# Performance work log

Hardware: AMD Instinct MI355X
Metric: run time of the kernel (lower is better)

The kernel has to match this reference:

```python
import jax, jax.numpy as jnp
import numpy as np

E = 512   # embed_dim
S = 16    # stat_dim
B = 2048  # batch
K = 64    # neighbors


def setup_inputs() -> dict:
    key = jax.random.key(0)
    ks = jax.random.split(key, 12)
    std_s1 = 1.0 / np.sqrt(3 * E + S)
    std_s2 = 1.0 / np.sqrt(E)
    std_p1 = 1.0 / np.sqrt(E + S)
    return {
        "query": jax.random.normal(ks[0], (B, E), jnp.float32),
        "condition": jax.random.normal(ks[1], (B, E), jnp.float32),
        "neighbors": jax.random.normal(ks[2], (B, K, E), jnp.float32),
        "neighbor_stats": jax.random.uniform(ks[3], (B, K, S), jnp.float32),
        # scorer: Linear(3E+S -> E), GELU, Linear(E -> 1)
        "sw1": jax.random.uniform(ks[4], (3 * E + S, E), jnp.float32, -std_s1, std_s1),
        "sb1": jax.random.uniform(ks[5], (E,), jnp.float32, -std_s1, std_s1),
        "sw2": jax.random.uniform(ks[6], (E, 1), jnp.float32, -std_s2, std_s2),
        "sb2": jax.random.uniform(ks[7], (1,), jnp.float32, -std_s2, std_s2),
        "sim_alpha": jnp.float32(1.0),
        # proj: Linear(E+S -> E), GELU, Linear(E -> E)
        "pw1": jax.random.uniform(ks[8], (E + S, E), jnp.float32, -std_p1, std_p1),
        "pb1": jax.random.uniform(ks[9], (E,), jnp.float32, -std_p1, std_p1),
        "pw2": jax.random.uniform(ks[10], (E, E), jnp.float32, -std_s2, std_s2),
        "pb2": jax.random.uniform(ks[11], (E,), jnp.float32, -std_s2, std_s2),
    }


def _gelu(x):
    return jax.nn.gelu(x, approximate=False)  # torch default GELU is exact erf


def reference(query, condition, neighbors, neighbor_stats,
              sw1, sb1, sw2, sb2, sim_alpha, pw1, pb1, pw2, pb2):
    b, k, e = neighbors.shape
    # broadcast query/condition over k and concat -> [B, K, 3E+S]
    q_rep = jnp.broadcast_to(query[:, None, :], (b, k, e))
    c_rep = jnp.broadcast_to(condition[:, None, :], (b, k, e))
    scorer_in = jnp.concatenate([q_rep, c_rep, neighbors, neighbor_stats], axis=-1)
    h = _gelu(scorer_in @ sw1 + sb1)          # dropout is identity in eval
    logits = (h @ sw2 + sb2)[..., 0]           # [B, K]
    sim_scores = neighbor_stats[..., -1]       # stat_dim > 0
    logits = logits + sim_alpha * sim_scores
    attn = jax.nn.softmax(logits, axis=-1)     # [B, K]
    nb_cat = jnp.concatenate([neighbors, neighbor_stats], axis=-1)  # [B, K, E+S]
    mixed = jnp.einsum('bk,bkd->bd', attn, nb_cat)
    out = _gelu(mixed @ pw1 + pb1) @ pw2 + pb2  # [B, E]
    return out, attn
```

## Files before the change

kernel.cpp:

```cpp
#include <hip/hip_runtime.h>

typedef _Float16 half_t;
typedef _Float16 half2_t __attribute__((ext_vector_type(2)));
typedef _Float16 half4_t __attribute__((ext_vector_type(4)));
typedef _Float16 half8_t __attribute__((ext_vector_type(8)));
typedef float floatx4 __attribute__((ext_vector_type(4)));
typedef float floatx16 __attribute__((ext_vector_type(16)));

#define NE 512
#define NS 16
#define NBATCH 2048
#define NK 64
#define AS 552

__device__ __forceinline__ float gelu_erf(float x) {
    float z = x * 0.70710678118654752440f;
    float az2 = z * z;
    float az = __builtin_fabsf(z);
    float t = __builtin_amdgcn_rcpf(__builtin_fmaf(0.3275911f, az, 1.0f));
    float p = __builtin_fmaf(1.061405429f, t, -1.453152027f);
    p = __builtin_fmaf(p, t, 1.421413741f);
    p = __builtin_fmaf(p, t, -0.284496736f);
    p = __builtin_fmaf(p, t, 0.254829592f);
    p = p * t;
    float e = __expf(-az2);
    float erfa = __builtin_fmaf(-p, e, 1.0f);
    unsigned int u = __float_as_uint(erfa) ^ (__float_as_uint(z) & 0x80000000u);
    return 0.5f * x * (1.0f + __uint_as_float(u));
}

__device__ __forceinline__ half4_t cvt4(float4 v) {
    return (half4_t){(half_t)v.x, (half_t)v.y, (half_t)v.z, (half_t)v.w};
}

__device__ __forceinline__ float colreduce16(const float (&x)[16], int lnb) {
    float y[8];
#pragma unroll
    for (int i = 0; i < 8; ++i) {
        float keep = (lnb & 1) ? x[2 * i + 1] : x[2 * i];
        float send = (lnb & 1) ? x[2 * i] : x[2 * i + 1];
        y[i] = keep + __shfl_xor(send, 1, 64);
    }
    float z[4];
#pragma unroll
    for (int i = 0; i < 4; ++i) {
        float keep = (lnb & 2) ? y[2 * i + 1] : y[2 * i];
        float send = (lnb & 2) ? y[2 * i] : y[2 * i + 1];
        z[i] = keep + __shfl_xor(send, 2, 64);
    }
    float u[2];
#pragma unroll
    for (int i = 0; i < 2; ++i) {
        float keep = (lnb & 4) ? z[2 * i + 1] : z[2 * i];
        float send = (lnb & 4) ? z[2 * i] : z[2 * i + 1];
        u[i] = keep + __shfl_xor(send, 4, 64);
    }
    float keep = (lnb & 8) ? u[1] : u[0];
    float send = (lnb & 8) ? u[0] : u[1];
    float v = keep + __shfl_xor(send, 8, 64);
    v += __shfl_xor(v, 16, 64);
    return v;
}

__device__ void pack_w_body(const float* __restrict__ src, half_t* __restrict__ dst,
                            int Ksrc, int t, int nb0, half_t* tile) {
    int tid = threadIdx.x;
#pragma unroll
    for (int i = 0; i < 8; ++i) {
        int idx = tid + i * 256;
        int kk = idx >> 6, np = idx & 63;
        int k = t * 32 + kk;
        float v = (k < Ksrc) ? src[(size_t)k * NE + nb0 + np] : 0.0f;
        tile[kk * 68 + np] = (half_t)v;
    }
    __syncthreads();
#pragma unroll
    for (int i = 0; i < 8; ++i) {
        int idx = tid + i * 256;
        int np = idx >> 5, kk = idx & 31;
        dst[((size_t)t * NE + nb0 + np) * 32 + kk] = tile[kk * 68 + np];
    }
}

__device__ void pack_w32_body(const float* __restrict__ src, half_t* __restrict__ dst,
                              int Ksrc, int t, int nb0, half_t* tile) {
    int tid = threadIdx.x;
#pragma unroll
    for (int i = 0; i < 4; ++i) {
        int idx = tid + i * 256;
        int kk = idx >> 6, n = idx & 63;
        int k = t * 16 + kk;
        float v = (k < Ksrc) ? src[(size_t)k * NE + nb0 + n] : 0.0f;
        tile[kk * 68 + n] = (half_t)v;
    }
    __syncthreads();
    int n = threadIdx.x >> 2, q = threadIdx.x & 3;
    half4_t h = {tile[(q * 4) * 68 + n], tile[(q * 4 + 1) * 68 + n],
                 tile[(q * 4 + 2) * 68 + n], tile[(q * 4 + 3) * 68 + n]};
    *(half4_t*)&dst[((size_t)t * NE + nb0 + n) * 16 + q * 4] = h;
}

__global__ __launch_bounds__(256) void pack_all(
    const float* __restrict__ sw1, const float* __restrict__ pw1,
    const float* __restrict__ pw2, half_t* __restrict__ Wq,
    half_t* __restrict__ Wns, half_t* __restrict__ Wp1, half_t* __restrict__ Wp2) {
    __shared__ half_t tile[32 * 68];
    int bx = blockIdx.x;
    if (bx < 256) {
        pack_w_body(sw1, Wq, 1024, bx >> 3, (bx & 7) * 64, tile);
    } else if (bx < 520) {
        int b2 = bx - 256;
        pack_w32_body(sw1 + (size_t)1024 * NE, Wns, 528, b2 >> 3, (b2 & 7) * 64, tile);
    } else if (bx < 656) {
        int b3 = bx - 520;
        pack_w_body(pw1, Wp1, 528, b3 >> 3, (b3 & 7) * 64, tile);
    } else {
        int b4 = bx - 656;
        pack_w_body(pw2, Wp2, 512, b4 >> 3, (b4 & 7) * 64, tile);
    }
}

__global__ __launch_bounds__(512) void qc_kernel(const float* __restrict__ q,
                                                 const float* __restrict__ c,
                                                 const half_t* __restrict__ Wq,
                                                 const float* __restrict__ sb1,
                                                 float* __restrict__ qcb) {
    constexpr int AS1 = 1032;
    __shared__ __align__(16) half_t A1[16 * AS1];
    int b0 = (blockIdx.x >> 1) * 16;
    int nh = (blockIdx.x & 1) * 256;
    int tid = threadIdx.x;
#pragma unroll
    for (int i = 0; i < 8; ++i) {
        int f = tid + i * 512;
        int row = f >> 8;
        int c4 = f & 255;
        const float* srcp = (c4 < 128) ? (q + (size_t)(b0 + row) * NE + c4 * 4)
                                       : (c + (size_t)(b0 + row) * NE + (c4 - 128) * 4);
        float4 v = *(const float4*)srcp;
        *(half4_t*)&A1[row * AS1 + c4 * 4] = cvt4(v);
    }
    __syncthreads();
    int w = tid >> 6, l = tid & 63, lg = l >> 4, ln = l & 15;
    floatx4 acc[2] = { {0,0,0,0}, {0,0,0,0} };
    for (int t = 0; t < 32; ++t) {
        half8_t a = *(const half8_t*)&A1[ln * AS1 + t * 32 + 8 * lg];
#pragma unroll
        for (int ni = 0; ni < 2; ++ni) {
            int n = nh + w * 32 + ni * 16 + ln;
            half8_t bf = *(const half8_t*)(Wq + ((size_t)t * NE + n) * 32 + 8 * lg);
            acc[ni] = __builtin_amdgcn_mfma_f32_16x16x32_f16(a, bf, acc[ni], 0, 0, 0);
        }
    }
#pragma unroll
    for (int ni = 0; ni < 2; ++ni) {
        int col = nh + w * 32 + ni * 16 + ln;
        float bias = sb1[col];
#pragma unroll
        for (int r = 0; r < 4; ++r) {
            int row = 4 * lg + r;
            qcb[(size_t)(b0 + row) * NE + col] = acc[ni][r] + bias;
        }
    }
}

__global__ __launch_bounds__(512, 4) void main_kernel(
    const float* __restrict__ neighbors, const float* __restrict__ stats,
    const half_t* __restrict__ Wns, const float* __restrict__ qcb,
    const float* __restrict__ sw2, const float* __restrict__ sb2,
    const float* __restrict__ alpha, float* __restrict__ attn_out,
    half_t* __restrict__ mixed) {
    __shared__ __align__(16) half_t A[64 * AS];
    __shared__ float Llds[64][17];
    __shared__ float attn_s[8][64];

    int b = blockIdx.x;
    int tid = threadIdx.x;
    const float* nb = neighbors + (size_t)b * NK * NE;
    const float* st = stats + (size_t)b * NK * NS;

    int r0 = tid >> 5;
    int c4 = tid & 31;
    int w = tid >> 6;
    int l = tid & 63, ln = l & 31, hi = l >> 5;
    const half_t* Abase = A + ln * AS + 8 * hi;
    const half_t* Wb = Wns + ((size_t)(w * 32 + ln)) * 16 + 8 * hi;

    float4 s0, s1, s2, s3, sst;
    float qv1, w21, qv2, w22;
    {
        float4 p0 = *(const float4*)(nb + (size_t)(r0) * NE + 4 * c4);
        float4 p1 = *(const float4*)(nb + (size_t)(r0 + 16) * NE + 4 * c4);
        float4 p2 = *(const float4*)(nb + (size_t)(r0 + 32) * NE + 4 * c4);
        float4 p3 = *(const float4*)(nb + (size_t)(r0 + 48) * NE + 4 * c4);
        __builtin_amdgcn_sched_barrier(0);
        s0 = *(const float4*)(nb + (size_t)(r0) * NE + 128 + 4 * c4);
        s1 = *(const float4*)(nb + (size_t)(r0 + 16) * NE + 128 + 4 * c4);
        s2 = *(const float4*)(nb + (size_t)(r0 + 32) * NE + 128 + 4 * c4);
        s3 = *(const float4*)(nb + (size_t)(r0 + 48) * NE + 128 + 4 * c4);
        qv1 = qcb[(size_t)b * NE + w * 32 + ln];
        w21 = sw2[w * 32 + ln];
        qv2 = qcb[(size_t)b * NE + 256 + w * 32 + ln];
        w22 = sw2[256 + w * 32 + ln];
        __builtin_amdgcn_sched_barrier(0);
        *(half4_t*)&A[(r0) * AS + 4 * c4] = cvt4(p0);
        *(half4_t*)&A[(r0 + 16) * AS + 4 * c4] = cvt4(p1);
        *(half4_t*)&A[(r0 + 32) * AS + 4 * c4] = cvt4(p2);
        *(half4_t*)&A[(r0 + 48) * AS + 4 * c4] = cvt4(p3);
    }
    asm volatile("s_waitcnt lgkmcnt(0)" ::: "memory");
    __builtin_amdgcn_sched_barrier(0);
    __builtin_amdgcn_s_barrier();
    __builtin_amdgcn_sched_barrier(0);

    floatx16 acc0 = {0,0,0,0,0,0,0,0,0,0,0,0,0,0,0,0};
    floatx16 acc1 = {0,0,0,0,0,0,0,0,0,0,0,0,0,0,0,0};

#pragma unroll 1
    for (int ch = 0; ch < 4; ++ch) {
        half8_t bfr[8];
#pragma unroll
        for (int s8 = 0; s8 < 8; ++s8)
            bfr[s8] = *(const half8_t*)(Wb + (size_t)(ch * 8 + s8) * 8192);
        __builtin_amdgcn_sched_barrier(0);
        float4 n0, n1, n2, n3;
        if (ch < 2) {
            n0 = *(const float4*)(nb + (size_t)(r0) * NE + (ch + 2) * 128 + 4 * c4);
            n1 = *(const float4*)(nb + (size_t)(r0 + 16) * NE + (ch + 2) * 128 + 4 * c4);
            n2 = *(const float4*)(nb + (size_t)(r0 + 32) * NE + (ch + 2) * 128 + 4 * c4);
            n3 = *(const float4*)(nb + (size_t)(r0 + 48) * NE + (ch + 2) * 128 + 4 * c4);
        } else if (ch == 2) {
            if (tid < 256)
                sst = *(const float4*)(st + (tid >> 2) * NS + (tid & 3) * 4);
        }
        __builtin_amdgcn_sched_barrier(0);
#pragma unroll
        for (int s8 = 0; s8 < 8; ++s8) {
            int col = ch * 128 + s8 * 16;
            half8_t a0 = *(const half8_t*)&Abase[col];
            half8_t a1 = *(const half8_t*)&Abase[32 * AS + col];
            acc0 = __builtin_amdgcn_mfma_f32_32x32x16_f16(a0, bfr[s8], acc0, 0, 0, 0);
            acc1 = __builtin_amdgcn_mfma_f32_32x32x16_f16(a1, bfr[s8], acc1, 0, 0, 0);
        }
        if (ch < 3) {
            *(half4_t*)&A[(r0) * AS + (ch + 1) * 128 + 4 * c4] = cvt4(s0);
            *(half4_t*)&A[(r0 + 16) * AS + (ch + 1) * 128 + 4 * c4] = cvt4(s1);
            *(half4_t*)&A[(r0 + 32) * AS + (ch + 1) * 128 + 4 * c4] = cvt4(s2);
            *(half4_t*)&A[(r0 + 48) * AS + (ch + 1) * 128 + 4 * c4] = cvt4(s3);
            s0 = n0; s1 = n1; s2 = n2; s3 = n3;
        } else {
            if (tid < 256)
                *(half4_t*)&A[(tid >> 2) * AS + 512 + (tid & 3) * 4] = cvt4(sst);
        }
        asm volatile("s_waitcnt lgkmcnt(0)" ::: "memory");
        __builtin_amdgcn_sched_barrier(0);
        __builtin_amdgcn_s_barrier();
        __builtin_amdgcn_sched_barrier(0);
    }
    {
        half8_t bfa = *(const half8_t*)(Wb + (size_t)32 * 8192);
        half8_t a0 = *(const half8_t*)&Abase[512];
        half8_t a1 = *(const half8_t*)&Abase[32 * AS + 512];
        acc0 = __builtin_amdgcn_mfma_f32_32x32x16_f16(a0, bfa, acc0, 0, 0, 0);
        acc1 = __builtin_amdgcn_mfma_f32_32x32x16_f16(a1, bfa, acc1, 0, 0, 0);
    }

    const half_t* Wb2 = Wb + 4096;
    half8_t pA0 = *(const half8_t*)(Wb2);
    half8_t pB0 = *(const half8_t*)(Wb2 + 8192);
    half8_t pA1 = *(const half8_t*)(Wb2 + 2 * 8192);
    half8_t pB1 = *(const half8_t*)(Wb2 + 3 * 8192);
    __builtin_amdgcn_sched_barrier(0);

    {
        float g0[16], g1[16];
#pragma unroll
        for (int r = 0; r < 16; ++r) {
            g0[r] = gelu_erf(acc0[r] + qv1) * w21;
            g1[r] = gelu_erf(acc1[r] + qv1) * w21;
        }
        float rA = colreduce16(g0, ln);
        float rB = colreduce16(g1, ln);
        if (ln < 16) {
            int row = (ln & 3) + 8 * (ln >> 2) + 4 * hi;
            Llds[row][w] = rA;
            Llds[32 + row][w] = rB;
        }
    }

    acc0 = (floatx16){0,0,0,0,0,0,0,0,0,0,0,0,0,0,0,0};
    acc1 = (floatx16){0,0,0,0,0,0,0,0,0,0,0,0,0,0,0,0};
#pragma unroll 1
    for (int t2 = 0; t2 < 16; ++t2) {
        int tn = 2 * t2 + 4;
        if (tn > 32) tn = 32;
        int tn1 = tn + 1;
        if (tn1 > 32) tn1 = 32;
        half8_t nA = *(const half8_t*)(Wb2 + (size_t)tn * 8192);
        half8_t nB = *(const half8_t*)(Wb2 + (size_t)tn1 * 8192);
        int col = t2 * 32;
        half8_t a0 = *(const half8_t*)&Abase[col];
        half8_t a1 = *(const half8_t*)&Abase[32 * AS + col];
        acc0 = __builtin_amdgcn_mfma_f32_32x32x16_f16(a0, pA0, acc0, 0, 0, 0);
        acc1 = __builtin_amdgcn_mfma_f32_32x32x16_f16(a1, pA0, acc1, 0, 0, 0);
        half8_t a0b = *(const half8_t*)&Abase[col + 16];
        half8_t a1b = *(const half8_t*)&Abase[32 * AS + col + 16];
        acc0 = __builtin_amdgcn_mfma_f32_32x32x16_f16(a0b, pB0, acc0, 0, 0, 0);
        acc1 = __builtin_amdgcn_mfma_f32_32x32x16_f16(a1b, pB0, acc1, 0, 0, 0);
        pA0 = pA1; pB0 = pB1; pA1 = nA; pB1 = nB;
    }
    {
        half8_t a0 = *(const half8_t*)&Abase[512];
        half8_t a1 = *(const half8_t*)&Abase[32 * AS + 512];
        acc0 = __builtin_amdgcn_mfma_f32_32x32x16_f16(a0, pA0, acc0, 0, 0, 0);
        acc1 = __builtin_amdgcn_mfma_f32_32x32x16_f16(a1, pA0, acc1, 0, 0, 0);
    }

    {
        float g0[16], g1[16];
#pragma unroll
        for (int r = 0; r < 16; ++r) {
            g0[r] = gelu_erf(acc0[r] + qv2) * w22;
            g1[r] = gelu_erf(acc1[r] + qv2) * w22;
        }
        float rA = colreduce16(g0, ln);
        float rB = colreduce16(g1, ln);
        if (ln < 16) {
            int row = (ln & 3) + 8 * (ln >> 2) + 4 * hi;
            Llds[row][8 + w] = rA;
            Llds[32 + row][8 + w] = rB;
        }
    }
    __syncthreads();

    {
        int k = l;
        float lsum = 0.0f;
#pragma unroll
        for (int j = 0; j < 16; ++j) lsum += Llds[k][j];
        float sim = st[k * NS + (NS - 1)];
        float logit = lsum + sb2[0] + alpha[0] * sim;
        float mx = logit;
#pragma unroll
        for (int m = 1; m < 64; m <<= 1) mx = fmaxf(mx, __shfl_xor(mx, m, 64));
        float e = __expf(logit - mx);
        float s = e;
#pragma unroll
        for (int m = 1; m < 64; m <<= 1) s += __shfl_xor(s, m, 64);
        float at = e / s;
        attn_s[w][k] = at;
        if (w == 0) attn_out[(size_t)b * NK + k] = at;
    }

    if (tid < 264) {
        int c0 = 2 * tid;
        float m0 = 0.0f, m1 = 0.0f;
#pragma unroll 8
        for (int k = 0; k < NK; ++k) {
            half2_t v = *(const half2_t*)&A[k * AS + c0];
            float aw = attn_s[w][k];
            m0 += aw * (float)v[0];
            m1 += aw * (float)v[1];
        }
        *(half2_t*)&mixed[(size_t)b * AS + c0] = (half2_t){(half_t)m0, (half_t)m1};
    } else if (tid < 270) {
        int z = tid - 264;
        half4_t hz = {};
        *(half4_t*)&mixed[(size_t)b * AS + 528 + 4 * z] = hz;
    }
}

__global__ __launch_bounds__(1024) void proj_kernel(
    const half_t* __restrict__ mixedp, const half_t* __restrict__ Wp1,
    const half_t* __restrict__ Wp2, const float* __restrict__ pb1,
    const float* __restrict__ pb2, float* __restrict__ out) {
    constexpr int AS3 = AS;
    __shared__ __align__(16) half_t A1[16 * AS3];
    int b0 = blockIdx.x * 16;
    int tid = threadIdx.x;
    const uint4* src = (const uint4*)(mixedp + (size_t)b0 * AS3);
    for (int i = tid; i < 1104; i += 1024) ((uint4*)A1)[i] = src[i];
    __syncthreads();

    int w = tid >> 6, l = tid & 63, lg = l >> 4, ln = l & 15;
    floatx4 acc[2] = { {0,0,0,0}, {0,0,0,0} };
    for (int t = 0; t < 17; ++t) {
        half8_t a = *(const half8_t*)&A1[ln * AS3 + t * 32 + 8 * lg];
#pragma unroll
        for (int ni = 0; ni < 2; ++ni) {
            int n = w * 32 + ni * 16 + ln;
            half8_t bf = *(const half8_t*)(Wp1 + ((size_t)t * NE + n) * 32 + 8 * lg);
            acc[ni] = __builtin_amdgcn_mfma_f32_16x16x32_f16(a, bf, acc[ni], 0, 0, 0);
        }
    }
    __syncthreads();
#pragma unroll
    for (int ni = 0; ni < 2; ++ni) {
        int col = w * 32 + ni * 16 + ln;
        float bias = pb1[col];
#pragma unroll
        for (int r = 0; r < 4; ++r) {
            int row = 4 * lg + r;
            A1[row * AS3 + col] = (half_t)gelu_erf(acc[ni][r] + bias);
        }
    }
    __syncthreads();
    floatx4 acc2[2] = { {0,0,0,0}, {0,0,0,0} };
    for (int t = 0; t < 16; ++t) {
        half8_t a = *(const half8_t*)&A1[ln * AS3 + t * 32 + 8 * lg];
#pragma unroll
        for (int ni = 0; ni < 2; ++ni) {
            int n = w * 32 + ni * 16 + ln;
            half8_t bf = *(const half8_t*)(Wp2 + ((size_t)t * NE + n) * 32 + 8 * lg);
            acc2[ni] = __builtin_amdgcn_mfma_f32_16x16x32_f16(a, bf, acc2[ni], 0, 0, 0);
        }
    }
#pragma unroll
    for (int ni = 0; ni < 2; ++ni) {
        int col = w * 32 + ni * 16 + ln;
        float bias = pb2[col];
#pragma unroll
        for (int r = 0; r < 4; ++r)
            out[(size_t)(b0 + 4 * lg + r) * NE + col] = acc2[ni][r] + bias;
    }
}

extern "C" void kernel_launch(void* const* d_in, const int* in_sizes, int n_in,
                              void* d_out, int out_size, void* d_ws, size_t ws_size,
                              hipStream_t stream) {
    (void)in_sizes; (void)n_in; (void)out_size; (void)ws_size;
    const float* q     = (const float*)d_in[0];
    const float* c     = (const float*)d_in[1];
    const float* nb    = (const float*)d_in[2];
    const float* st    = (const float*)d_in[3];
    const float* sw1   = (const float*)d_in[4];
    const float* sb1   = (const float*)d_in[5];
    const float* sw2   = (const float*)d_in[6];
    const float* sb2   = (const float*)d_in[7];
    const float* alpha = (const float*)d_in[8];
    const float* pw1   = (const float*)d_in[9];
    const float* pb1   = (const float*)d_in[10];
    const float* pw2   = (const float*)d_in[11];
    const float* pb2   = (const float*)d_in[12];

    char* ws = (char*)d_ws;
    half_t* Wq  = (half_t*)(ws + 0);
    half_t* Wns = (half_t*)(ws + 1048576);
    half_t* Wp1 = (half_t*)(ws + 1605632);
    half_t* Wp2 = (half_t*)(ws + 2162688);
    float*  qcb = (float*)(ws + 2686976);
    half_t* mix = (half_t*)(ws + 6881280);

    float* outp  = (float*)d_out;
    float* attnp = outp + (size_t)NBATCH * NE;

    pack_all<<<784, 256, 0, stream>>>(sw1, pw1, pw2, Wq, Wns, Wp1, Wp2);
    qc_kernel<<<256, 512, 0, stream>>>(q, c, Wq, sb1, qcb);
    main_kernel<<<2048, 512, 0, stream>>>(nb, st, Wns, qcb, sw2, sb2, alpha, attnp, mix);
    proj_kernel<<<128, 1024, 0, stream>>>(mix, Wp1, Wp2, pb1, pb2, outp);
}
```

Before: 171.0 us.

## Double-buffer neighbor chunks in LDS and re-stream neighbors to cut LDS footprint

Replaces the full 64x552 half tile in shared memory with two 128-column chunk buffers plus a small stats buffer, and raises the launch-bounds minimum from 4 to 6 blocks. With the smaller footprint more blocks should fit per CU. The price is that neighbor rows are re-read from global memory for the second GEMM half and again, as fp32, for the attention-weighted mix, which now broadcasts weights with shuffles. This roughly triples neighbor traffic, relying on cache hits. The tighter launch bound may also force register spills.

```diff
diff --git a/kernel.cpp b/kernel.cpp
--- a/kernel.cpp
+++ b/kernel.cpp
@@ -12,6 +12,8 @@
 #define NBATCH 2048
 #define NK 64
 #define AS 552
+#define CH_AS 136
+#define ST_AS 40
 
 __device__ __forceinline__ float gelu_erf(float x) {
     float z = x * 0.70710678118654752440f;
@@ -164,15 +166,15 @@
     }
 }
 
-__global__ __launch_bounds__(512, 4) void main_kernel(
+__global__ __launch_bounds__(512, 6) void main_kernel(
     const float* __restrict__ neighbors, const float* __restrict__ stats,
     const half_t* __restrict__ Wns, const float* __restrict__ qcb,
     const float* __restrict__ sw2, const float* __restrict__ sb2,
     const float* __restrict__ alpha, float* __restrict__ attn_out,
     half_t* __restrict__ mixed) {
-    __shared__ __align__(16) half_t A[64 * AS];
+    __shared__ __align__(16) half_t Abuf[2][64 * CH_AS];
+    __shared__ __align__(16) half_t Ast[64 * ST_AS];
     __shared__ float Llds[64][17];
-    __shared__ float attn_s[8][64];
 
     int b = blockIdx.x;
     int tid = threadIdx.x;
@@ -183,30 +185,30 @@
     int c4 = tid & 31;
     int w = tid >> 6;
     int l = tid & 63, ln = l & 31, hi = l >> 5;
-    const half_t* Abase = A + ln * AS + 8 * hi;
     const half_t* Wb = Wns + ((size_t)(w * 32 + ln)) * 16 + 8 * hi;
 
     float4 s0, s1, s2, s3, sst;
     float qv1, w21, qv2, w22;
+
     {
         float4 p0 = *(const float4*)(nb + (size_t)(r0) * NE + 4 * c4);
         float4 p1 = *(const float4*)(nb + (size_t)(r0 + 16) * NE + 4 * c4);
         float4 p2 = *(const float4*)(nb + (size_t)(r0 + 32) * NE + 4 * c4);
         float4 p3 = *(const float4*)(nb + (size_t)(r0 + 48) * NE + 4 * c4);
+        qv1 = qcb[(size_t)b * NE + w * 32 + ln];
+        w21 = sw2[w * 32 + ln];
+        qv2 = qcb[(size_t)b * NE + 256 + w * 32 + ln];
+        w22 = sw2[256 + w * 32 + ln];
+        __builtin_amdgcn_sched_barrier(0);
+        *(half4_t*)&Abuf[0][(r0) * CH_AS + 4 * c4] = cvt4(p0);
+        *(half4_t*)&Abuf[0][(r0 + 16) * CH_AS + 4 * c4] = cvt4(p1);
+        *(half4_t*)&Abuf[0][(r0 + 32) * CH_AS + 4 * c4] = cvt4(p2);
+        *(half4_t*)&Abuf[0][(r0 + 48) * CH_AS + 4 * c4] = cvt4(p3);
         __builtin_amdgcn_sched_barrier(0);
         s0 = *(const float4*)(nb + (size_t)(r0) * NE + 128 + 4 * c4);
         s1 = *(const float4*)(nb + (size_t)(r0 + 16) * NE + 128 + 4 * c4);
         s2 = *(const float4*)(nb + (size_t)(r0 + 32) * NE + 128 + 4 * c4);
         s3 = *(const float4*)(nb + (size_t)(r0 + 48) * NE + 128 + 4 * c4);
-        qv1 = qcb[(size_t)b * NE + w * 32 + ln];
-        w21 = sw2[w * 32 + ln];
-        qv2 = qcb[(size_t)b * NE + 256 + w * 32 + ln];
-        w22 = sw2[256 + w * 32 + ln];
-        __builtin_amdgcn_sched_barrier(0);
-        *(half4_t*)&A[(r0) * AS + 4 * c4] = cvt4(p0);
-        *(half4_t*)&A[(r0 + 16) * AS + 4 * c4] = cvt4(p1);
-        *(half4_t*)&A[(r0 + 32) * AS + 4 * c4] = cvt4(p2);
-        *(half4_t*)&A[(r0 + 48) * AS + 4 * c4] = cvt4(p3);
     }
     asm volatile("s_waitcnt lgkmcnt(0)" ::: "memory");
     __builtin_amdgcn_sched_barrier(0);
@@ -223,35 +225,39 @@
         for (int s8 = 0; s8 < 8; ++s8)
             bfr[s8] = *(const half8_t*)(Wb + (size_t)(ch * 8 + s8) * 8192);
         __builtin_amdgcn_sched_barrier(0);
-        float4 n0, n1, n2, n3;
+        const half_t* Ab = Abuf[ch & 1] + ln * CH_AS + 8 * hi;
+#pragma unroll
+        for (int s8 = 0; s8 < 8; ++s8) {
+            half8_t a0 = *(const half8_t*)&Ab[s8 * 16];
+            half8_t a1 = *(const half8_t*)&Ab[32 * CH_AS + s8 * 16];
+            acc0 = __builtin_amdgcn_mfma_f32_32x32x16_f16(a0, bfr[s8], acc0, 0, 0, 0);
+            acc1 = __builtin_amdgcn_mfma_f32_32x32x16_f16(a1, bfr[s8], acc1, 0, 0, 0);
+        }
+        __builtin_amdgcn_sched_barrier(0);
+        if (ch < 3) {
+            half_t* Aw = Abuf[(ch + 1) & 1];
+            *(half4_t*)&Aw[(r0) * CH_AS + 4 * c4] = cvt4(s0);
+            *(half4_t*)&Aw[(r0 + 16) * CH_AS + 4 * c4] = cvt4(s1);
+            *(half4_t*)&Aw[(r0 + 32) * CH_AS + 4 * c4] = cvt4(s2);
+            *(half4_t*)&Aw[(r0 + 48) * CH_AS + 4 * c4] = cvt4(s3);
+        } else {
+            if (tid < 256)
+                *(half4_t*)&Ast[(tid >> 2) * ST_AS + (tid & 3) * 4] = cvt4(sst);
+        }
+        __builtin_amdgcn_sched_barrier(0);
         if (ch < 2) {
-            n0 = *(const float4*)(nb + (size_t)(r0) * NE + (ch + 2) * 128 + 4 * c4);
-            n1 = *(const float4*)(nb + (size_t)(r0 + 16) * NE + (ch + 2) * 128 + 4 * c4);
-            n2 = *(const float4*)(nb + (size_t)(r0 + 32) * NE + (ch + 2) * 128 + 4 * c4);
-            n3 = *(const float4*)(nb + (size_t)(r0 + 48) * NE + (ch + 2) * 128 + 4 * c4);
+            s0 = *(const float4*)(nb + (size_t)(r0) * NE + (ch + 2) * 128 + 4 * c4);
+            s1 = *(const float4*)(nb + (size_t)(r0 + 16) * NE + (ch + 2) * 128 + 4 * c4);
+            s2 = *(const float4*)(nb + (size_t)(r0 + 32) * NE + (ch + 2) * 128 + 4 * c4);
+            s3 = *(const float4*)(nb + (size_t)(r0 + 48) * NE + (ch + 2) * 128 + 4 * c4);
         } else if (ch == 2) {
+            s0 = *(const float4*)(nb + (size_t)(r0) * NE + 4 * c4);
+            s1 = *(const float4*)(nb + (size_t)(r0 + 16) * NE + 4 * c4);
+            s2 = *(const float4*)(nb + (size_t)(r0 + 32) * NE + 4 * c4);
+            s3 = *(const float4*)(nb + (size_t)(r0 + 48) * NE + 4 * c4);
             if (tid < 256)
                 sst = *(const float4*)(st + (tid >> 2) * NS + (tid & 3) * 4);
         }
-        __builtin_amdgcn_sched_barrier(0);
-#pragma unroll
-        for (int s8 = 0; s8 < 8; ++s8) {
-            int col = ch * 128 + s8 * 16;
-            half8_t a0 = *(const half8_t*)&Abase[col];
-            half8_t a1 = *(const half8_t*)&Abase[32 * AS + col];
-            acc0 = __builtin_amdgcn_mfma_f32_32x32x16_f16(a0, bfr[s8], acc0, 0, 0, 0);
-            acc1 = __builtin_amdgcn_mfma_f32_32x32x16_f16(a1, bfr[s8], acc1, 0, 0, 0);
-        }
-        if (ch < 3) {
-            *(half4_t*)&A[(r0) * AS + (ch + 1) * 128 + 4 * c4] = cvt4(s0);
-            *(half4_t*)&A[(r0 + 16) * AS + (ch + 1) * 128 + 4 * c4] = cvt4(s1);
-            *(half4_t*)&A[(r0 + 32) * AS + (ch + 1) * 128 + 4 * c4] = cvt4(s2);
-            *(half4_t*)&A[(r0 + 48) * AS + (ch + 1) * 128 + 4 * c4] = cvt4(s3);
-            s0 = n0; s1 = n1; s2 = n2; s3 = n3;
-        } else {
-            if (tid < 256)
-                *(half4_t*)&A[(tid >> 2) * AS + 512 + (tid & 3) * 4] = cvt4(sst);
-        }
         asm volatile("s_waitcnt lgkmcnt(0)" ::: "memory");
         __builtin_amdgcn_sched_barrier(0);
         __builtin_amdgcn_s_barrier();
@@ -259,17 +265,25 @@
     }
     {
         half8_t bfa = *(const half8_t*)(Wb + (size_t)32 * 8192);
-        half8_t a0 = *(const half8_t*)&Abase[512];
-        half8_t a1 = *(const half8_t*)&Abase[32 * AS + 512];
+        const half_t* Asb = Ast + ln * ST_AS + 8 * hi;
+        half8_t a0 = *(const half8_t*)&Asb[0];
+        half8_t a1 = *(const half8_t*)&Asb[32 * ST_AS];
         acc0 = __builtin_amdgcn_mfma_f32_32x32x16_f16(a0, bfa, acc0, 0, 0, 0);
         acc1 = __builtin_amdgcn_mfma_f32_32x32x16_f16(a1, bfa, acc1, 0, 0, 0);
     }
 
-    const half_t* Wb2 = Wb + 4096;
-    half8_t pA0 = *(const half8_t*)(Wb2);
-    half8_t pB0 = *(const half8_t*)(Wb2 + 8192);
-    half8_t pA1 = *(const half8_t*)(Wb2 + 2 * 8192);
-    half8_t pB1 = *(const half8_t*)(Wb2 + 3 * 8192);
+    {
+        half_t* Aw = Abuf[0];
+        *(half4_t*)&Aw[(r0) * CH_AS + 4 * c4] = cvt4(s0);
+        *(half4_t*)&Aw[(r0 + 16) * CH_AS + 4 * c4] = cvt4(s1);
+        *(half4_t*)&Aw[(r0 + 32) * CH_AS + 4 * c4] = cvt4(s2);
+        *(half4_t*)&Aw[(r0 + 48) * CH_AS + 4 * c4] = cvt4(s3);
+    }
+    __builtin_amdgcn_sched_barrier(0);
+    s0 = *(const float4*)(nb + (size_t)(r0) * NE + 128 + 4 * c4);
+    s1 = *(const float4*)(nb + (size_t)(r0 + 16) * NE + 128 + 4 * c4);
+    s2 = *(const float4*)(nb + (size_t)(r0 + 32) * NE + 128 + 4 * c4);
+    s3 = *(const float4*)(nb + (size_t)(r0 + 48) * NE + 128 + 4 * c4);
     __builtin_amdgcn_sched_barrier(0);
 
     {
@@ -287,33 +301,56 @@
             Llds[32 + row][w] = rB;
         }
     }
+    asm volatile("s_waitcnt lgkmcnt(0)" ::: "memory");
+    __builtin_amdgcn_sched_barrier(0);
+    __builtin_amdgcn_s_barrier();
+    __builtin_amdgcn_sched_barrier(0);
 
     acc0 = (floatx16){0,0,0,0,0,0,0,0,0,0,0,0,0,0,0,0};
     acc1 = (floatx16){0,0,0,0,0,0,0,0,0,0,0,0,0,0,0,0};
+    const half_t* Wb2 = Wb + 4096;
 #pragma unroll 1
-    for (int t2 = 0; t2 < 16; ++t2) {
-        int tn = 2 * t2 + 4;
-        if (tn > 32) tn = 32;
-        int tn1 = tn + 1;
-        if (tn1 > 32) tn1 = 32;
-        half8_t nA = *(const half8_t*)(Wb2 + (size_t)tn * 8192);
-        half8_t nB = *(const half8_t*)(Wb2 + (size_t)tn1 * 8192);
-        int col = t2 * 32;
-        half8_t a0 = *(const half8_t*)&Abase[col];
-        half8_t a1 = *(const half8_t*)&Abase[32 * AS + col];
-        acc0 = __builtin_amdgcn_mfma_f32_32x32x16_f16(a0, pA0, acc0, 0, 0, 0);
-        acc1 = __builtin_amdgcn_mfma_f32_32x32x16_f16(a1, pA0, acc1, 0, 0, 0);
-        half8_t a0b = *(const half8_t*)&Abase[col + 16];
-        half8_t a1b = *(const half8_t*)&Abase[32 * AS + col + 16];
-        acc0 = __builtin_amdgcn_mfma_f32_32x32x16_f16(a0b, pB0, acc0, 0, 0, 0);
-        acc1 = __builtin_amdgcn_mfma_f32_32x32x16_f16(a1b, pB0, acc1, 0, 0, 0);
-        pA0 = pA1; pB0 = pB1; pA1 = nA; pB1 = nB;
-    }
-    {
-        half8_t a0 = *(const half8_t*)&Abase[512];
-        half8_t a1 = *(const half8_t*)&Abase[32 * AS + 512];
-        acc0 = __builtin_amdgcn_mfma_f32_32x32x16_f16(a0, pA0, acc0, 0, 0, 0);
-        acc1 = __builtin_amdgcn_mfma_f32_32x32x16_f16(a1, pA0, acc1, 0, 0, 0);
+    for (int ch = 0; ch < 4; ++ch) {
+        half8_t bfr[8];
+#pragma unroll
+        for (int s8 = 0; s8 < 8; ++s8)
+            bfr[s8] = *(const half8_t*)(Wb2 + (size_t)(ch * 8 + s8) * 8192);
+        __builtin_amdgcn_sched_barrier(0);
+        const half_t* Ab = Abuf[ch & 1] + ln * CH_AS + 8 * hi;
+#pragma unroll
+        for (int s8 = 0; s8 < 8; ++s8) {
+            half8_t a0 = *(const half8_t*)&Ab[s8 * 16];
+            half8_t a1 = *(const half8_t*)&Ab[32 * CH_AS + s8 * 16];
+            acc0 = __builtin_amdgcn_mfma_f32_32x32x16_f16(a0, bfr[s8], acc0, 0, 0, 0);
+            acc1 = __builtin_amdgcn_mfma_f32_32x32x16_f16(a1, bfr[s8], acc1, 0, 0, 0);
+        }
+        __builtin_amdgcn_sched_barrier(0);
+        if (ch < 3) {
+            half_t* Aw = Abuf[(ch + 1) & 1];
+            *(half4_t*)&Aw[(r0) * CH_AS + 4 * c4] = cvt4(s0);
+            *(half4_t*)&Aw[(r0 + 16) * CH_AS + 4 * c4] = cvt4(s1);
+            *(half4_t*)&Aw[(r0 + 32) * CH_AS + 4 * c4] = cvt4(s2);
+            *(half4_t*)&Aw[(r0 + 48) * CH_AS + 4 * c4] = cvt4(s3);
+            __builtin_amdgcn_sched_barrier(0);
+            if (ch < 2) {
+                s0 = *(const float4*)(nb + (size_t)(r0) * NE + (ch + 2) * 128 + 4 * c4);
+                s1 = *(const float4*)(nb + (size_t)(r0 + 16) * NE + (ch + 2) * 128 + 4 * c4);
+                s2 = *(const float4*)(nb + (size_t)(r0 + 32) * NE + (ch + 2) * 128 + 4 * c4);
+                s3 = *(const float4*)(nb + (size_t)(r0 + 48) * NE + (ch + 2) * 128 + 4 * c4);
+            }
+            asm volatile("s_waitcnt lgkmcnt(0)" ::: "memory");
+            __builtin_amdgcn_sched_barrier(0);
+            __builtin_amdgcn_s_barrier();
+            __builtin_amdgcn_sched_barrier(0);
+        }
+    }
+    {
+        half8_t bfa = *(const half8_t*)(Wb2 + (size_t)32 * 8192);
+        const half_t* Asb = Ast + ln * ST_AS + 8 * hi;
+        half8_t a0 = *(const half8_t*)&Asb[0];
+        half8_t a1 = *(const half8_t*)&Asb[32 * ST_AS];
+        acc0 = __builtin_amdgcn_mfma_f32_32x32x16_f16(a0, bfa, acc0, 0, 0, 0);
+        acc1 = __builtin_amdgcn_mfma_f32_32x32x16_f16(a1, bfa, acc1, 0, 0, 0);
     }
 
     {
@@ -333,6 +370,7 @@
     }
     __syncthreads();
 
+    float at;
     {
         int k = l;
         float lsum = 0.0f;
@@ -347,26 +385,30 @@
         float s = e;
 #pragma unroll
         for (int m = 1; m < 64; m <<= 1) s += __shfl_xor(s, m, 64);
-        float at = e / s;
-        attn_s[w][k] = at;
-        if (w == 0) attn_out[(size_t)b * NK + k] = at;
-    }
-
-    if (tid < 264) {
-        int c0 = 2 * tid;
-        float m0 = 0.0f, m1 = 0.0f;
+        at = e / s;
+        if (w == 0) {
+            attn_out[(size_t)b * NK + l] = at;
+            Llds[l][16] = at;
+        }
+    }
+
+    {
+        float m0 = 0.0f;
 #pragma unroll 8
         for (int k = 0; k < NK; ++k) {
-            half2_t v = *(const half2_t*)&A[k * AS + c0];
-            float aw = attn_s[w][k];
-            m0 += aw * (float)v[0];
-            m1 += aw * (float)v[1];
-        }
-        *(half2_t*)&mixed[(size_t)b * AS + c0] = (half2_t){(half_t)m0, (half_t)m1};
-    } else if (tid < 270) {
-        int z = tid - 264;
-        half4_t hz = {};
-        *(half4_t*)&mixed[(size_t)b * AS + 528 + 4 * z] = hz;
+            float aw = __shfl(at, k, 64);
+            m0 += aw * nb[(size_t)k * NE + tid];
+        }
+        mixed[(size_t)b * AS + tid] = (half_t)m0;
+        if (tid < 16) {
+            float ms = 0.0f;
+#pragma unroll
+            for (int k = 0; k < NK; ++k)
+                ms += Llds[k][16] * (float)Ast[k * ST_AS + tid];
+            mixed[(size_t)b * AS + 512 + tid] = (half_t)ms;
+        } else if (tid < 40) {
+            mixed[(size_t)b * AS + 528 + (tid - 16)] = (half_t)0.0f;
+        }
     }
 }
 
```

New measurement: 348.6 us. 2.04x slower.

## Compute both scorer column halves in a single K pass with four accumulators

Applied to the files above, without the earlier changes.

Each wave now owns 64 contiguous output columns and computes them with four 32x32 accumulators in one sweep over K, where before it made two sequential passes over the A tile with two accumulators each. Each A fragment read from LDS now feeds four MFMAs instead of two, halving LDS reads of A. Weight fragments are prefetched through a rotating 4-slot register ring, and the neighbor chunk for the next step is loaded at the top of each iteration. The cost is more accumulator and weight registers, which may limit occupancy or cause spills.

```diff
diff --git a/kernel.cpp b/kernel.cpp
--- a/kernel.cpp
+++ b/kernel.cpp
@@ -184,24 +184,27 @@
     int w = tid >> 6;
     int l = tid & 63, ln = l & 31, hi = l >> 5;
     const half_t* Abase = A + ln * AS + 8 * hi;
-    const half_t* Wb = Wns + ((size_t)(w * 32 + ln)) * 16 + 8 * hi;
-
-    float4 s0, s1, s2, s3, sst;
-    float qv1, w21, qv2, w22;
+    const half_t* WbA = Wns + ((size_t)(w * 64 + ln)) * 16 + 8 * hi;
+    const half_t* WbB = WbA + 32 * 16;
+
+    float4 s0, s1, s2, s3;
+    float qvA, wA, qvB, wB;
+    half8_t bfA[4], bfB[4];
+
     {
         float4 p0 = *(const float4*)(nb + (size_t)(r0) * NE + 4 * c4);
         float4 p1 = *(const float4*)(nb + (size_t)(r0 + 16) * NE + 4 * c4);
         float4 p2 = *(const float4*)(nb + (size_t)(r0 + 32) * NE + 4 * c4);
         float4 p3 = *(const float4*)(nb + (size_t)(r0 + 48) * NE + 4 * c4);
-        __builtin_amdgcn_sched_barrier(0);
-        s0 = *(const float4*)(nb + (size_t)(r0) * NE + 128 + 4 * c4);
-        s1 = *(const float4*)(nb + (size_t)(r0 + 16) * NE + 128 + 4 * c4);
-        s2 = *(const float4*)(nb + (size_t)(r0 + 32) * NE + 128 + 4 * c4);
-        s3 = *(const float4*)(nb + (size_t)(r0 + 48) * NE + 128 + 4 * c4);
-        qv1 = qcb[(size_t)b * NE + w * 32 + ln];
-        w21 = sw2[w * 32 + ln];
-        qv2 = qcb[(size_t)b * NE + 256 + w * 32 + ln];
-        w22 = sw2[256 + w * 32 + ln];
+        qvA = qcb[(size_t)b * NE + w * 64 + ln];
+        wA = sw2[w * 64 + ln];
+        qvB = qcb[(size_t)b * NE + w * 64 + 32 + ln];
+        wB = sw2[w * 64 + 32 + ln];
+#pragma unroll
+        for (int s = 0; s < 4; ++s) {
+            bfA[s] = *(const half8_t*)(WbA + (size_t)s * 8192);
+            bfB[s] = *(const half8_t*)(WbB + (size_t)s * 8192);
+        }
         __builtin_amdgcn_sched_barrier(0);
         *(half4_t*)&A[(r0) * AS + 4 * c4] = cvt4(p0);
         *(half4_t*)&A[(r0 + 16) * AS + 4 * c4] = cvt4(p1);
@@ -213,122 +216,103 @@
     __builtin_amdgcn_s_barrier();
     __builtin_amdgcn_sched_barrier(0);
 
-    floatx16 acc0 = {0,0,0,0,0,0,0,0,0,0,0,0,0,0,0,0};
-    floatx16 acc1 = {0,0,0,0,0,0,0,0,0,0,0,0,0,0,0,0};
+    floatx16 acc00 = {0,0,0,0,0,0,0,0,0,0,0,0,0,0,0,0};
+    floatx16 acc01 = {0,0,0,0,0,0,0,0,0,0,0,0,0,0,0,0};
+    floatx16 acc10 = {0,0,0,0,0,0,0,0,0,0,0,0,0,0,0,0};
+    floatx16 acc11 = {0,0,0,0,0,0,0,0,0,0,0,0,0,0,0,0};
 
 #pragma unroll 1
-    for (int ch = 0; ch < 4; ++ch) {
-        half8_t bfr[8];
-#pragma unroll
-        for (int s8 = 0; s8 < 8; ++s8)
-            bfr[s8] = *(const half8_t*)(Wb + (size_t)(ch * 8 + s8) * 8192);
-        __builtin_amdgcn_sched_barrier(0);
-        float4 n0, n1, n2, n3;
-        if (ch < 2) {
-            n0 = *(const float4*)(nb + (size_t)(r0) * NE + (ch + 2) * 128 + 4 * c4);
-            n1 = *(const float4*)(nb + (size_t)(r0 + 16) * NE + (ch + 2) * 128 + 4 * c4);
-            n2 = *(const float4*)(nb + (size_t)(r0 + 32) * NE + (ch + 2) * 128 + 4 * c4);
-            n3 = *(const float4*)(nb + (size_t)(r0 + 48) * NE + (ch + 2) * 128 + 4 * c4);
-        } else if (ch == 2) {
-            if (tid < 256)
-                sst = *(const float4*)(st + (tid >> 2) * NS + (tid & 3) * 4);
-        }
+    for (int ch = 0; ch < 3; ++ch) {
+        s0 = *(const float4*)(nb + (size_t)(r0) * NE + (ch + 1) * 128 + 4 * c4);
+        s1 = *(const float4*)(nb + (size_t)(r0 + 16) * NE + (ch + 1) * 128 + 4 * c4);
+        s2 = *(const float4*)(nb + (size_t)(r0 + 32) * NE + (ch + 1) * 128 + 4 * c4);
+        s3 = *(const float4*)(nb + (size_t)(r0 + 48) * NE + (ch + 1) * 128 + 4 * c4);
         __builtin_amdgcn_sched_barrier(0);
 #pragma unroll
         for (int s8 = 0; s8 < 8; ++s8) {
+            const int slot = s8 & 3;
+            half8_t bA = bfA[slot], bB = bfB[slot];
+            bfA[slot] = *(const half8_t*)(WbA + (size_t)(ch * 8 + s8 + 4) * 8192);
+            bfB[slot] = *(const half8_t*)(WbB + (size_t)(ch * 8 + s8 + 4) * 8192);
             int col = ch * 128 + s8 * 16;
             half8_t a0 = *(const half8_t*)&Abase[col];
             half8_t a1 = *(const half8_t*)&Abase[32 * AS + col];
-            acc0 = __builtin_amdgcn_mfma_f32_32x32x16_f16(a0, bfr[s8], acc0, 0, 0, 0);
-            acc1 = __builtin_amdgcn_mfma_f32_32x32x16_f16(a1, bfr[s8], acc1, 0, 0, 0);
-        }
-        if (ch < 3) {
-            *(half4_t*)&A[(r0) * AS + (ch + 1) * 128 + 4 * c4] = cvt4(s0);
-            *(half4_t*)&A[(r0 + 16) * AS + (ch + 1) * 128 + 4 * c4] = cvt4(s1);
-            *(half4_t*)&A[(r0 + 32) * AS + (ch + 1) * 128 + 4 * c4] = cvt4(s2);
-            *(half4_t*)&A[(r0 + 48) * AS + (ch + 1) * 128 + 4 * c4] = cvt4(s3);
-            s0 = n0; s1 = n1; s2 = n2; s3 = n3;
-        } else {
-            if (tid < 256)
-                *(half4_t*)&A[(tid >> 2) * AS + 512 + (tid & 3) * 4] = cvt4(sst);
-        }
+            acc00 = __builtin_amdgcn_mfma_f32_32x32x16_f16(a0, bA, acc00, 0, 0, 0);
+            acc10 = __builtin_amdgcn_mfma_f32_32x32x16_f16(a1, bA, acc10, 0, 0, 0);
+            acc01 = __builtin_amdgcn_mfma_f32_32x32x16_f16(a0, bB, acc01, 0, 0, 0);
+            acc11 = __builtin_amdgcn_mfma_f32_32x32x16_f16(a1, bB, acc11, 0, 0, 0);
+        }
+        __builtin_amdgcn_sched_barrier(0);
+        *(half4_t*)&A[(r0) * AS + (ch + 1) * 128 + 4 * c4] = cvt4(s0);
+        *(half4_t*)&A[(r0 + 16) * AS + (ch + 1) * 128 + 4 * c4] = cvt4(s1);
+        *(half4_t*)&A[(r0 + 32) * AS + (ch + 1) * 128 + 4 * c4] = cvt4(s2);
+        *(half4_t*)&A[(r0 + 48) * AS + (ch + 1) * 128 + 4 * c4] = cvt4(s3);
         asm volatile("s_waitcnt lgkmcnt(0)" ::: "memory");
         __builtin_amdgcn_sched_barrier(0);
         __builtin_amdgcn_s_barrier();
         __builtin_amdgcn_sched_barrier(0);
     }
+
     {
-        half8_t bfa = *(const half8_t*)(Wb + (size_t)32 * 8192);
-        half8_t a0 = *(const half8_t*)&Abase[512];
-        half8_t a1 = *(const half8_t*)&Abase[32 * AS + 512];
-        acc0 = __builtin_amdgcn_mfma_f32_32x32x16_f16(a0, bfa, acc0, 0, 0, 0);
-        acc1 = __builtin_amdgcn_mfma_f32_32x32x16_f16(a1, bfa, acc1, 0, 0, 0);
-    }
-
-    const half_t* Wb2 = Wb + 4096;
-    half8_t pA0 = *(const half8_t*)(Wb2);
-    half8_t pB0 = *(const half8_t*)(Wb2 + 8192);
-    half8_t pA1 = *(const half8_t*)(Wb2 + 2 * 8192);
-    half8_t pB1 = *(const half8_t*)(Wb2 + 3 * 8192);
-    __builtin_amdgcn_sched_barrier(0);
-
-    {
-        float g0[16], g1[16];
-#pragma unroll
-        for (int r = 0; r < 16; ++r) {
-            g0[r] = gelu_erf(acc0[r] + qv1) * w21;
-            g1[r] = gelu_erf(acc1[r] + qv1) * w21;
-        }
-        float rA = colreduce16(g0, ln);
-        float rB = colreduce16(g1, ln);
-        if (ln < 16) {
-            int row = (ln & 3) + 8 * (ln >> 2) + 4 * hi;
-            Llds[row][w] = rA;
-            Llds[32 + row][w] = rB;
-        }
-    }
-
-    acc0 = (floatx16){0,0,0,0,0,0,0,0,0,0,0,0,0,0,0,0};
-    acc1 = (floatx16){0,0,0,0,0,0,0,0,0,0,0,0,0,0,0,0};
-#pragma unroll 1
-    for (int t2 = 0; t2 < 16; ++t2) {
-        int tn = 2 * t2 + 4;
-        if (tn > 32) tn = 32;
-        int tn1 = tn + 1;
-        if (tn1 > 32) tn1 = 32;
-        half8_t nA = *(const half8_t*)(Wb2 + (size_t)tn * 8192);
-        half8_t nB = *(const half8_t*)(Wb2 + (size_t)tn1 * 8192);
-        int col = t2 * 32;
-        half8_t a0 = *(const half8_t*)&Abase[col];
-        half8_t a1 = *(const half8_t*)&Abase[32 * AS + col];
-        acc0 = __builtin_amdgcn_mfma_f32_32x32x16_f16(a0, pA0, acc0, 0, 0, 0);
-        acc1 = __builtin_amdgcn_mfma_f32_32x32x16_f16(a1, pA0, acc1, 0, 0, 0);
-        half8_t a0b = *(const half8_t*)&Abase[col + 16];
-        half8_t a1b = *(const half8_t*)&Abase[32 * AS + col + 16];
-        acc0 = __builtin_amdgcn_mfma_f32_32x32x16_f16(a0b, pB0, acc0, 0, 0, 0);
-        acc1 = __builtin_amdgcn_mfma_f32_32x32x16_f16(a1b, pB0, acc1, 0, 0, 0);
-        pA0 = pA1; pB0 = pB1; pA1 = nA; pB1 = nB;
+        if (tid < 256)
+            s0 = *(const float4*)(st + (tid >> 2) * NS + (tid & 3) * 4);
+        __builtin_amdgcn_sched_barrier(0);
+#pragma unroll
+        for (int s8 = 0; s8 < 8; ++s8) {
+            const int slot = s8 & 3;
+            half8_t bA = bfA[slot], bB = bfB[slot];
+            if (s8 <= 4) {
+                bfA[slot] = *(const half8_t*)(WbA + (size_t)(28 + s8) * 8192);
+                bfB[slot] = *(const half8_t*)(WbB + (size_t)(28 + s8) * 8192);
+            }
+            int col = 3 * 128 + s8 * 16;
+            half8_t a0 = *(const half8_t*)&Abase[col];
+            half8_t a1 = *(const half8_t*)&Abase[32 * AS + col];
+            acc00 = __builtin_amdgcn_mfma_f32_32x32x16_f16(a0, bA, acc00, 0, 0, 0);
+            acc10 = __builtin_amdgcn_mfma_f32_32x32x16_f16(a1, bA, acc10, 0, 0, 0);
+            acc01 = __builtin_amdgcn_mfma_f32_32x32x16_f16(a0, bB, acc01, 0, 0, 0);
+            acc11 = __builtin_amdgcn_mfma_f32_32x32x16_f16(a1, bB, acc11, 0, 0, 0);
+        }
+        __builtin_amdgcn_sched_barrier(0);
+        if (tid < 256)
+            *(half4_t*)&A[(tid >> 2) * AS + 512 + (tid & 3) * 4] = cvt4(s0);
+        asm volatile("s_waitcnt lgkmcnt(0)" ::: "memory");
+        __builtin_amdgcn_sched_barrier(0);
+        __builtin_amdgcn_s_barrier();
+        __builtin_amdgcn_sched_barrier(0);
     }
     {
         half8_t a0 = *(const half8_t*)&Abase[512];
         half8_t a1 = *(const half8_t*)&Abase[32 * AS + 512];
-        acc0 = __builtin_amdgcn_mfma_f32_32x32x16_f16(a0, pA0, acc0, 0, 0, 0);
-        acc1 = __builtin_amdgcn_mfma_f32_32x32x16_f16(a1, pA0, acc1, 0, 0, 0);
+        acc00 = __builtin_amdgcn_mfma_f32_32x32x16_f16(a0, bfA[0], acc00, 0, 0, 0);
+        acc10 = __builtin_amdgcn_mfma_f32_32x32x16_f16(a1, bfA[0], acc10, 0, 0, 0);
+        acc01 = __builtin_amdgcn_mfma_f32_32x32x16_f16(a0, bfB[0], acc01, 0, 0, 0);
+        acc11 = __builtin_amdgcn_mfma_f32_32x32x16_f16(a1, bfB[0], acc11, 0, 0, 0);
     }
 
     {
-        float g0[16], g1[16];
-#pragma unroll
-        for (int r = 0; r < 16; ++r) {
-            g0[r] = gelu_erf(acc0[r] + qv2) * w22;
-            g1[r] = gelu_erf(acc1[r] + qv2) * w22;
-        }
+        float g0[16];
+#pragma unroll
+        for (int r = 0; r < 16; ++r) g0[r] = gelu_erf(acc00[r] + qvA) * wA;
         float rA = colreduce16(g0, ln);
-        float rB = colreduce16(g1, ln);
+#pragma unroll
+        for (int r = 0; r < 16; ++r) g0[r] = gelu_erf(acc01[r] + qvB) * wB;
+        float rB = colreduce16(g0, ln);
         if (ln < 16) {
             int row = (ln & 3) + 8 * (ln >> 2) + 4 * hi;
-            Llds[row][8 + w] = rA;
-            Llds[32 + row][8 + w] = rB;
+            Llds[row][2 * w] = rA;
+            Llds[row][2 * w + 1] = rB;
+        }
+#pragma unroll
+        for (int r = 0; r < 16; ++r) g0[r] = gelu_erf(acc10[r] + qvA) * wA;
+        rA = colreduce16(g0, ln);
+#pragma unroll
+        for (int r = 0; r < 16; ++r) g0[r] = gelu_erf(acc11[r] + qvB) * wB;
+        rB = colreduce16(g0, ln);
+        if (ln < 16) {
+            int row = (ln & 3) + 8 * (ln >> 2) + 4 * hi;
+            Llds[32 + row][2 * w] = rA;
+            Llds[32 + row][2 * w + 1] = rB;
         }
     }
     __syncthreads();
```

Result: slower. 182.6 us (+6.8%).
